# Kernel optimization log

Measured on AMD Instinct MI355X. Metric: run time of the kernel, lower is better.

## Reference

```python
import jax, jax.numpy as jnp
import numpy as np


def setup_inputs() -> dict:
    key = jax.random.key(0)
    k1, k2 = jax.random.split(key)
    Xc = jax.random.normal(k1, (16384, 3), dtype=jnp.float32)
    Xt = jax.random.normal(k2, (16384, 3), dtype=jnp.float32)
    return {"Xc": Xc, "Xt": Xt}


def _sq_dists(Xc, Xt):
    # squared Euclidean distances [N, M] via the gram trick (matches cdist(p=2)**2)
    x2 = jnp.sum(Xc * Xc, axis=-1)  # [N]
    y2 = jnp.sum(Xt * Xt, axis=-1)  # [M]
    d2 = x2[:, None] + y2[None, :] - 2.0 * (Xc @ Xt.T)
    return jnp.maximum(d2, 0.0)


def reference(Xc, Xt):
    dists = _sq_dists(Xc, Xt)              # [N, M]
    min_dist_Xc = jnp.min(dists, axis=1)   # [N]
    min_dist_Xt = jnp.min(dists, axis=0)   # [M]
    return jnp.mean(min_dist_Xc) + jnp.mean(min_dist_Xt)
```

## Files before the change

### kernel.cpp

```cpp
#include <hip/hip_runtime.h>

#define BLOCK    256
#define DC       8
#define CHUNKPTS 2048
#define STAGEPTS 512
#define NSTAGE   (CHUNKPTS / STAGEPTS)
#define NQ       16384

typedef _Float16 f16;
typedef __attribute__((ext_vector_type(8)))  _Float16 f16x8;
typedef __attribute__((ext_vector_type(16))) float    f32x16;

union Pack { f16 h[16]; uint4 u[2]; };
union U8   { uint4 u; f16x8 v; };

__device__ __forceinline__ void split(float v, f16& h, f16& l) {
    h = (f16)v;
    l = (f16)(v - (float)h);
}

__device__ __forceinline__ Pack pack_db(float x, float y, float z) {
    f16 hx, lx, hy, ly, hz, lz, nh, nl;
    split(x, hx, lx); split(y, hy, ly); split(z, hz, lz);
    float n2 = fmaf(x, x, fmaf(y, y, z * z));
    split(n2, nh, nl);
    Pack p;
    p.h[0] = hx;  p.h[1] = hy;  p.h[2] = hz;
    p.h[3] = lx;  p.h[4] = ly;  p.h[5] = lz;
    p.h[6] = hx;  p.h[7] = hy;  p.h[8] = hz;
    p.h[9] = lx;  p.h[10] = ly; p.h[11] = lz;
    p.h[12] = nh; p.h[13] = nl; p.h[14] = (f16)0.f; p.h[15] = (f16)0.f;
    return p;
}

__device__ __forceinline__ Pack pack_q(float x, float y, float z) {
    f16 hx, lx, hy, ly, hz, lz;
    split(-2.f * x, hx, lx); split(-2.f * y, hy, ly); split(-2.f * z, hz, lz);
    Pack p;
    p.h[0] = hx; p.h[1] = hy; p.h[2] = hz;
    p.h[3] = hx; p.h[4] = hy; p.h[5] = hz;
    p.h[6] = lx; p.h[7] = ly; p.h[8] = lz;
    p.h[9] = lx; p.h[10] = ly; p.h[11] = lz;
    p.h[12] = (f16)1.f; p.h[13] = (f16)1.f; p.h[14] = (f16)0.f; p.h[15] = (f16)0.f;
    return p;
}

__global__ __launch_bounds__(BLOCK) void chamfer_pass(
    const float* __restrict__ Xc, const float* __restrict__ Xt,
    float* __restrict__ part, float* __restrict__ out)
{
    __shared__ uint4 tile[STAGEPTS * 2];

    const int tid = threadIdx.x;
    if (blockIdx.x == 0 && blockIdx.y == 0 && blockIdx.z == 0 && tid == 0)
        out[0] = 0.0f;

    const float* Xq = (blockIdx.z == 0) ? Xc : Xt;
    const float* Xd = (blockIdx.z == 0) ? Xt : Xc;

    const int lane = tid & 63;
    const int w    = tid >> 6;
    const int col  = lane & 31;
    const int ksel = lane >> 5;

    const int qrowbase = blockIdx.x * BLOCK + w * 64;
    f16x8 a0, a1;
    {
        int r0 = qrowbase + col;
        Pack p0 = pack_q(Xq[3 * r0], Xq[3 * r0 + 1], Xq[3 * r0 + 2]);
        U8 s; s.u = ksel ? p0.u[1] : p0.u[0]; a0 = s.v;
        int r1 = r0 + 32;
        Pack p1 = pack_q(Xq[3 * r1], Xq[3 * r1 + 1], Xq[3 * r1 + 2]);
        s.u = ksel ? p1.u[1] : p1.u[0]; a1 = s.v;
    }

    f32x16 acc0, acc1, zacc;
#pragma unroll
    for (int r = 0; r < 16; ++r) { acc0[r] = 3.0e38f; acc1[r] = 3.0e38f; zacc[r] = 0.f; }

    const int dbase = blockIdx.y * CHUNKPTS;
    const char* ldsb = (const char*)tile + (col * 32 + ksel * 16);

    for (int s = 0; s < NSTAGE; ++s) {
        __syncthreads();
        {
            const float* src = Xd + (size_t)(dbase + s * STAGEPTS) * 3;
#pragma unroll
            for (int c = 0; c < 2; ++c) {
                int p = tid + c * BLOCK;
                Pack pb = pack_db(src[3 * p], src[3 * p + 1], src[3 * p + 2]);
                tile[2 * p]     = pb.u[0];
                tile[2 * p + 1] = pb.u[1];
            }
        }
        __syncthreads();

#pragma unroll
        for (int bt = 0; bt < 16; bt += 2) {
            f16x8 b0 = *(const f16x8*)(ldsb + bt * 1024);
            f16x8 b1 = *(const f16x8*)(ldsb + bt * 1024 + 1024);
            f32x16 d0 = __builtin_amdgcn_mfma_f32_32x32x16_f16(a0, b0, zacc, 0, 0, 0);
            f32x16 d1 = __builtin_amdgcn_mfma_f32_32x32x16_f16(a0, b1, zacc, 0, 0, 0);
#pragma unroll
            for (int r = 0; r < 16; ++r)
                acc0[r] = fminf(fminf(d0[r], d1[r]), acc0[r]);
            f32x16 e0 = __builtin_amdgcn_mfma_f32_32x32x16_f16(a1, b0, zacc, 0, 0, 0);
            f32x16 e1 = __builtin_amdgcn_mfma_f32_32x32x16_f16(a1, b1, zacc, 0, 0, 0);
#pragma unroll
            for (int r = 0; r < 16; ++r)
                acc1[r] = fminf(fminf(e0[r], e1[r]), acc1[r]);
        }
    }

#pragma unroll
    for (int r = 0; r < 16; ++r) {
        float v0 = acc0[r], v1 = acc1[r];
#pragma unroll
        for (int off = 1; off < 32; off <<= 1) {
            v0 = fminf(v0, __shfl_xor(v0, off, 64));
            v1 = fminf(v1, __shfl_xor(v1, off, 64));
        }
        if (col == 0) {
            int row = (r & 3) + 8 * (r >> 2) + 4 * ksel;
            int q0  = qrowbase + row;
            part[((size_t)blockIdx.z * NQ + q0) * DC + blockIdx.y]      = v0;
            part[((size_t)blockIdx.z * NQ + q0 + 32) * DC + blockIdx.y] = v1;
        }
    }
}

__global__ __launch_bounds__(BLOCK) void chamfer_reduce(
    const float* __restrict__ part, const float* __restrict__ Xc,
    const float* __restrict__ Xt, float* __restrict__ out)
{
    __shared__ float red[4];
    int e = blockIdx.x * BLOCK + threadIdx.x;

    const float4* pb = (const float4*)(part + (size_t)e * DC);
    float4 m0 = pb[0], m1 = pb[1];
    float mn = fminf(fminf(fminf(m0.x, m0.y), fminf(m0.z, m0.w)),
                     fminf(fminf(m1.x, m1.y), fminf(m1.z, m1.w)));

    const float* X = (e < NQ) ? Xc : Xt;
    int q = (e < NQ) ? e : e - NQ;
    float x = X[3 * q], y = X[3 * q + 1], z = X[3 * q + 2];
    float n2 = fmaf(x, x, fmaf(y, y, z * z));
    float s = fmaxf(mn + n2, 0.0f) * (1.0f / 16384.0f);

#pragma unroll
    for (int off = 32; off > 0; off >>= 1) s += __shfl_down(s, off, 64);
    int wv = threadIdx.x >> 6, ln = threadIdx.x & 63;
    if (ln == 0) red[wv] = s;
    __syncthreads();
    if (threadIdx.x == 0) atomicAdd(out, red[0] + red[1] + red[2] + red[3]);
}

extern "C" void kernel_launch(void* const* d_in, const int* in_sizes, int n_in,
                              void* d_out, int out_size, void* d_ws, size_t ws_size,
                              hipStream_t stream) {
    const float* Xc = (const float*)d_in[0];
    const float* Xt = (const float*)d_in[1];
    float* part = (float*)d_ws;
    float* out  = (float*)d_out;

    dim3 grid(NQ / BLOCK , DC, 2);
    chamfer_pass<<<grid, BLOCK, 0, stream>>>(Xc, Xt, part, out);
    chamfer_reduce<<<(2 * NQ) / BLOCK , BLOCK, 0, stream>>>(part, Xc, Xt, out);
}
```

Baseline: 87.39 us.

## Precompute packed fp16 split operands in a prep kernel and stream B from global

```diff
diff --git a/kernel.cpp b/kernel.cpp
--- a/kernel.cpp
+++ b/kernel.cpp
@@ -3,8 +3,6 @@
 #define BLOCK    256
 #define DC       8
 #define CHUNKPTS 2048
-#define STAGEPTS 512
-#define NSTAGE   (CHUNKPTS / STAGEPTS)
 #define NQ       16384
 
 typedef _Float16 f16;
@@ -45,71 +43,68 @@
     return p;
 }
 
+__global__ __launch_bounds__(BLOCK) void chamfer_prep(
+    const float* __restrict__ Xc, const float* __restrict__ Xt,
+    uint4* __restrict__ Ac, uint4* __restrict__ At,
+    uint4* __restrict__ Bc, uint4* __restrict__ Bt,
+    float* __restrict__ out)
+{
+    int i = blockIdx.x * BLOCK + threadIdx.x;
+    if (i == 0) out[0] = 0.0f;
+    float x = Xc[3 * i], y = Xc[3 * i + 1], z = Xc[3 * i + 2];
+    Pack a = pack_q(x, y, z), b = pack_db(x, y, z);
+    Ac[2 * i] = a.u[0]; Ac[2 * i + 1] = a.u[1];
+    Bc[2 * i] = b.u[0]; Bc[2 * i + 1] = b.u[1];
+    x = Xt[3 * i]; y = Xt[3 * i + 1]; z = Xt[3 * i + 2];
+    a = pack_q(x, y, z); b = pack_db(x, y, z);
+    At[2 * i] = a.u[0]; At[2 * i + 1] = a.u[1];
+    Bt[2 * i] = b.u[0]; Bt[2 * i + 1] = b.u[1];
+}
+
 __global__ __launch_bounds__(BLOCK) void chamfer_pass(
-    const float* __restrict__ Xc, const float* __restrict__ Xt,
-    float* __restrict__ part, float* __restrict__ out)
+    const uint4* __restrict__ Ac, const uint4* __restrict__ At,
+    const uint4* __restrict__ Bc, const uint4* __restrict__ Bt,
+    float* __restrict__ part)
 {
-    __shared__ uint4 tile[STAGEPTS * 2];
-
-    const int tid = threadIdx.x;
-    if (blockIdx.x == 0 && blockIdx.y == 0 && blockIdx.z == 0 && tid == 0)
-        out[0] = 0.0f;
-
-    const float* Xq = (blockIdx.z == 0) ? Xc : Xt;
-    const float* Xd = (blockIdx.z == 0) ? Xt : Xc;
-
+    const int tid  = threadIdx.x;
     const int lane = tid & 63;
     const int w    = tid >> 6;
     const int col  = lane & 31;
     const int ksel = lane >> 5;
 
-    const int qrowbase = blockIdx.x * BLOCK + w * 64;
+    const uint4* Aq = blockIdx.z ? At : Ac;
+    const uint4* Bd = blockIdx.z ? Bc : Bt;
+
+    const int qw = blockIdx.x * BLOCK + w * 64;
     f16x8 a0, a1;
     {
-        int r0 = qrowbase + col;
-        Pack p0 = pack_q(Xq[3 * r0], Xq[3 * r0 + 1], Xq[3 * r0 + 2]);
-        U8 s; s.u = ksel ? p0.u[1] : p0.u[0]; a0 = s.v;
-        int r1 = r0 + 32;
-        Pack p1 = pack_q(Xq[3 * r1], Xq[3 * r1 + 1], Xq[3 * r1 + 2]);
-        s.u = ksel ? p1.u[1] : p1.u[0]; a1 = s.v;
+        U8 u;
+        u.u = Aq[(qw + col) * 2 + ksel];      a0 = u.v;
+        u.u = Aq[(qw + 32 + col) * 2 + ksel]; a1 = u.v;
     }
 
     f32x16 acc0, acc1, zacc;
 #pragma unroll
     for (int r = 0; r < 16; ++r) { acc0[r] = 3.0e38f; acc1[r] = 3.0e38f; zacc[r] = 0.f; }
 
-    const int dbase = blockIdx.y * CHUNKPTS;
-    const char* ldsb = (const char*)tile + (col * 32 + ksel * 16);
+    const uint4* bbase = Bd + (size_t)blockIdx.y * (CHUNKPTS * 2) + (col * 2 + ksel);
 
-    for (int s = 0; s < NSTAGE; ++s) {
-        __syncthreads();
-        {
-            const float* src = Xd + (size_t)(dbase + s * STAGEPTS) * 3;
+#pragma unroll 4
+    for (int g = 0; g < 64; g += 2) {
+        U8 u0, u1;
+        u0.u = bbase[(g    ) * 64];
+        u1.u = bbase[(g + 1) * 64];
+        f16x8 b0 = u0.v, b1 = u1.v;
+        f32x16 d0 = __builtin_amdgcn_mfma_f32_32x32x16_f16(a0, b0, zacc, 0, 0, 0);
+        f32x16 d1 = __builtin_amdgcn_mfma_f32_32x32x16_f16(a0, b1, zacc, 0, 0, 0);
 #pragma unroll
-            for (int c = 0; c < 2; ++c) {
-                int p = tid + c * BLOCK;
-                Pack pb = pack_db(src[3 * p], src[3 * p + 1], src[3 * p + 2]);
-                tile[2 * p]     = pb.u[0];
-                tile[2 * p + 1] = pb.u[1];
-            }
-        }
-        __syncthreads();
-
+        for (int r = 0; r < 16; ++r)
+            acc0[r] = fminf(fminf(d0[r], d1[r]), acc0[r]);
+        f32x16 e0 = __builtin_amdgcn_mfma_f32_32x32x16_f16(a1, b0, zacc, 0, 0, 0);
+        f32x16 e1 = __builtin_amdgcn_mfma_f32_32x32x16_f16(a1, b1, zacc, 0, 0, 0);
 #pragma unroll
-        for (int bt = 0; bt < 16; bt += 2) {
-            f16x8 b0 = *(const f16x8*)(ldsb + bt * 1024);
-            f16x8 b1 = *(const f16x8*)(ldsb + bt * 1024 + 1024);
-            f32x16 d0 = __builtin_amdgcn_mfma_f32_32x32x16_f16(a0, b0, zacc, 0, 0, 0);
-            f32x16 d1 = __builtin_amdgcn_mfma_f32_32x32x16_f16(a0, b1, zacc, 0, 0, 0);
-#pragma unroll
-            for (int r = 0; r < 16; ++r)
-                acc0[r] = fminf(fminf(d0[r], d1[r]), acc0[r]);
-            f32x16 e0 = __builtin_amdgcn_mfma_f32_32x32x16_f16(a1, b0, zacc, 0, 0, 0);
-            f32x16 e1 = __builtin_amdgcn_mfma_f32_32x32x16_f16(a1, b1, zacc, 0, 0, 0);
-#pragma unroll
-            for (int r = 0; r < 16; ++r)
-                acc1[r] = fminf(fminf(e0[r], e1[r]), acc1[r]);
-        }
+        for (int r = 0; r < 16; ++r)
+            acc1[r] = fminf(fminf(e0[r], e1[r]), acc1[r]);
     }
 
 #pragma unroll
@@ -122,7 +117,7 @@
         }
         if (col == 0) {
             int row = (r & 3) + 8 * (r >> 2) + 4 * ksel;
-            int q0  = qrowbase + row;
+            int q0  = qw + row;
             part[((size_t)blockIdx.z * NQ + q0) * DC + blockIdx.y]      = v0;
             part[((size_t)blockIdx.z * NQ + q0 + 32) * DC + blockIdx.y] = v1;
         }
@@ -160,10 +155,18 @@
                               hipStream_t stream) {
     const float* Xc = (const float*)d_in[0];
     const float* Xt = (const float*)d_in[1];
-    float* part = (float*)d_ws;
-    float* out  = (float*)d_out;
+    float* out = (float*)d_out;
+
+    uint4* Ac = (uint4*)d_ws;
+    uint4* At = Ac + 2 * NQ;
+    uint4* Bc = At + 2 * NQ;
+    uint4* Bt = Bc + 2 * NQ;
+    float* part = (float*)(Bt + 2 * NQ);
+
+    chamfer_prep<<<NQ / BLOCK, BLOCK, 0, stream>>>(Xc, Xt, Ac, At, Bc, Bt, out);
 
     dim3 grid(NQ / BLOCK , DC, 2);
-    chamfer_pass<<<grid, BLOCK, 0, stream>>>(Xc, Xt, part, out);
-    chamfer_reduce<<<(2 * NQ) / BLOCK , BLOCK, 0, stream>>>(part, Xc, Xt, out);
+    chamfer_pass<<<grid, BLOCK, 0, stream>>>(Ac, At, Bc, Bt, part);
+
+    chamfer_reduce<<<(2 * NQ) / BLOCK, BLOCK, 0, stream>>>(part, Xc, Xt, out);
 }
```

Measured after the change: 90.78 us. +3.9%, slower.
